# Performance work log

Measured on AMD Instinct MI355X. Metric: run time of the kernel, lower is better.

Reference implementation:

```python
import jax, jax.numpy as jnp
import numpy as np

N_NODES = 50000
N_EDGES = 800000
D = 128  # node_feat_size == edge_hidden_size


def setup_inputs() -> dict:
    key = jax.random.key(0)
    ks = jax.random.split(key, 10)
    return {
        "edge_logits": jax.random.normal(ks[0], (N_EDGES, 1), jnp.float32),
        "node_feats": jax.random.normal(ks[1], (N_NODES, D), jnp.float32),
        "src": jax.random.randint(ks[2], (N_EDGES,), 0, N_NODES),
        "dst": jax.random.randint(ks[3], (N_EDGES,), 0, N_NODES),
        "W_proj": jax.random.normal(ks[4], (D, D), jnp.float32) * 0.05,
        "b_proj": jax.random.normal(ks[5], (D,), jnp.float32) * 0.05,
        "W_ih": jax.random.normal(ks[6], (3 * D, D), jnp.float32) * 0.05,
        "b_ih": jax.random.normal(ks[7], (3 * D,), jnp.float32) * 0.05,
        "W_hh": jax.random.normal(ks[8], (3 * D, D), jnp.float32) * 0.05,
        "b_hh": jax.random.normal(ks[9], (3 * D,), jnp.float32) * 0.05,
    }


def reference(edge_logits, node_feats, src, dst, W_proj, b_proj, W_ih, b_ih, W_hh, b_hh):
    N = node_feats.shape[0]
    # --- edge softmax: normalize logits over incoming edges of each dst node ---
    emax = jax.ops.segment_max(edge_logits, dst, num_segments=N)      # [N,1]
    ex = jnp.exp(edge_logits - emax[dst])                             # [E,1]
    esum = jax.ops.segment_sum(ex, dst, num_segments=N)               # [N,1]
    a = ex / esum[dst]                                                # [E,1]
    # --- project nodes (dropout=0 -> identity), gather-multiply-scatter ---
    hv = node_feats @ W_proj.T + b_proj                               # [N,D]
    msg = hv[src] * a                                                 # [E,D]
    c = jax.ops.segment_sum(msg, dst, num_segments=N)                 # [N,D]
    context = jax.nn.elu(c)
    # --- GRUCell(input=context, hidden=node_feats), torch semantics ---
    gi = context @ W_ih.T + b_ih                                      # [N,3D]
    gh = node_feats @ W_hh.T + b_hh                                   # [N,3D]
    i_r, i_z, i_n = jnp.split(gi, 3, axis=-1)
    h_r, h_z, h_n = jnp.split(gh, 3, axis=-1)
    r = jax.nn.sigmoid(i_r + h_r)
    z = jax.nn.sigmoid(i_z + h_z)
    n = jnp.tanh(i_n + r * h_n)
    h_new = (1.0 - z) * n + z * node_feats
    return jax.nn.relu(h_new)
```

## Files before the change

### kernel.cpp

```cpp
#include <hip/hip_runtime.h>
#include <hip/hip_fp16.h>
#include <math.h>

#define NN 50000
#define NE 800000
#define DD 128
#define SLOT 64
#define NXCD 8
#define DRANGE 6250
#define FILLB 1568
#define WPREP 578
#define NFCONV 6250

typedef short bf16x8 __attribute__((ext_vector_type(8)));
typedef float f32x4 __attribute__((ext_vector_type(4)));

#define GLOAD_LDS16(gp, lp) \
    __builtin_amdgcn_global_load_lds((const __attribute__((address_space(1))) void*)(gp), \
                                     (__attribute__((address_space(3))) void*)(lp), 16, 0, 0)

__device__ __forceinline__ unsigned short f2bf(float x) {
    unsigned u = __float_as_uint(x);
    unsigned r = (u + 0x7FFFu + ((u >> 16) & 1u)) >> 16;
    return (unsigned short)r;
}
__device__ __forceinline__ float bf2f(unsigned short b) {
    return __uint_as_float(((unsigned)b) << 16);
}
__device__ __forceinline__ unsigned pack2(float x, float y) {
    return (unsigned)f2bf(x) | ((unsigned)f2bf(y) << 16);
}
__device__ __forceinline__ unsigned short f2h(float x) {
    _Float16 h = (_Float16)x;
    return *reinterpret_cast<unsigned short*>(&h);
}
__device__ __forceinline__ float h2f(unsigned short u) {
    _Float16 h = *reinterpret_cast<_Float16*>(&u);
    return (float)h;
}
__device__ __forceinline__ float fsig(float x) { return 1.f / (1.f + __expf(-x)); }
__device__ __forceinline__ float ftanh(float x) { return 1.f - 2.f / (__expf(2.f * x) + 1.f); }

__device__ __forceinline__ float wbig_val(const float* Wih, const float* Whh, int r, int c) {
    if (r < 256)  return (c < 128) ? Wih[r * 128 + c] : Whh[r * 128 + (c - 128)];
    if (r < 384)  return (c < 128) ? Wih[r * 128 + c] : 0.f;
    return (c < 128) ? 0.f : Whh[(r - 128) * 128 + (c - 128)];
}

__device__ __forceinline__ void fill_one(const float* __restrict__ logits,
                                         const int* __restrict__ src,
                                         int* __restrict__ cnt,
                                         unsigned* __restrict__ csr,
                                         int e, int d) {
    unsigned v = (unsigned)(unsigned short)src[e] |
                 ((unsigned)f2h(__expf(logits[e])) << 16);
    int p = atomicAdd(&cnt[d], 1);
    if (p < SLOT) csr[(size_t)d * SLOT + p] = v;
}

__global__ __launch_bounds__(256) void k_prepfill(const float* __restrict__ logits,
                                                  const int* __restrict__ src,
                                                  const int* __restrict__ dst,
                                                  int* __restrict__ cnt,
                                                  unsigned* __restrict__ csr,
                                                  const float* __restrict__ Wp,
                                                  const float* __restrict__ Wih,
                                                  const float* __restrict__ bih,
                                                  const float* __restrict__ Whh,
                                                  const float* __restrict__ bhh,
                                                  const float* __restrict__ nf,
                                                  unsigned short* __restrict__ Wfrag,
                                                  unsigned short* __restrict__ Wpfrag,
                                                  float* __restrict__ bbig,
                                                  unsigned* __restrict__ nfb) {
    if (blockIdx.x < FILLB) {
        const int g = blockIdx.x & 7;
        const int chunk = blockIdx.x >> 3;
        const int dlo = g * DRANGE;
        const int dhi = min(dlo + DRANGE, NN);
#pragma unroll
        for (int i = 0; i < 4; i++) {
            int e4 = chunk * 4096 + i * 1024 + (int)threadIdx.x * 4;
            if (e4 + 3 < NE) {
                int4 d = *(const int4*)(dst + e4);
                if (d.x >= dlo && d.x < dhi) fill_one(logits, src, cnt, csr, e4 + 0, d.x);
                if (d.y >= dlo && d.y < dhi) fill_one(logits, src, cnt, csr, e4 + 1, d.y);
                if (d.z >= dlo && d.z < dhi) fill_one(logits, src, cnt, csr, e4 + 2, d.z);
                if (d.w >= dlo && d.w < dhi) fill_one(logits, src, cnt, csr, e4 + 3, d.w);
            } else {
                for (int k = 0; k < 4; k++) {
                    int e = e4 + k;
                    if (e < NE) {
                        int dd = dst[e];
                        if (dd >= dlo && dd < dhi) fill_one(logits, src, cnt, csr, e, dd);
                    }
                }
            }
        }
    } else if (blockIdx.x < FILLB + WPREP) {
        int idx = (blockIdx.x - FILLB) * 256 + threadIdx.x;
        if (idx < 512 * 256) {
            int e = idx & 7, lane = (idx >> 3) & 63, ct = (idx >> 9) & 31, ks = idx >> 14;
            int r = ct * 16 + (lane & 15);
            int k = ks * 32 + (lane >> 4) * 8 + e;
            Wfrag[idx] = f2bf(wbig_val(Wih, Whh, r, k));
        } else if (idx < 512 * 256 + 128 * 128) {
            int i = idx - 512 * 256;
            int e = i & 7, lane = (i >> 3) & 63, ct = (i >> 9) & 7, ks = i >> 12;
            int r = ct * 16 + (lane & 15);
            int k = ks * 32 + (lane >> 4) * 8 + e;
            Wpfrag[i] = f2bf(Wp[r * 128 + k]);
        } else if (idx < 512 * 256 + 128 * 128 + 512) {
            int j = idx - (512 * 256 + 128 * 128);
            float v;
            if (j < 256)      v = bih[j] + bhh[j];
            else if (j < 384) v = bih[j];
            else              v = bhh[j - 128];
            bbig[j] = v;
        }
    } else {
        int t = (blockIdx.x - FILLB - WPREP) * 256 + threadIdx.x;
        float4 v = ((const float4*)nf)[t];
        nfb[t * 2 + 0] = pack2(v.x, v.y);
        nfb[t * 2 + 1] = pack2(v.z, v.w);
    }
}

__global__ __launch_bounds__(256, 2) void k_proj(const unsigned short* __restrict__ nfb,
                                                 const unsigned short* __restrict__ Wpfrag,
                                                 const float* __restrict__ bp,
                                                 unsigned short* __restrict__ hvb) {
    __shared__ unsigned short Bs[2][8 * 64 * 8];
    const int t = threadIdx.x;
    const int w = t >> 6;
    const int lane = t & 63;
    const int row0 = blockIdx.x * 64 + w * 16;
    const int rowA = min(row0 + (lane & 15), NN - 1);
    const int koff = (lane >> 4) * 8;

    bf16x8 a[4];
#pragma unroll
    for (int ks = 0; ks < 4; ks++)
        a[ks] = *reinterpret_cast<const bf16x8*>(nfb + (size_t)rowA * DD + ks * 32 + koff);

    f32x4 acc[8];
#pragma unroll
    for (int i = 0; i < 8; i++) acc[i] = (f32x4){0.f, 0.f, 0.f, 0.f};

#pragma unroll
    for (int i = 0; i < 2; i++)
        GLOAD_LDS16(Wpfrag + (size_t)(i * 256 + t) * 8, &Bs[0][(i * 256 + t) * 8]);
    __syncthreads();

#pragma unroll
    for (int ks = 0; ks < 4; ks++) {
        const int cur = ks & 1;
        if (ks < 3) {
#pragma unroll
            for (int i = 0; i < 2; i++)
                GLOAD_LDS16(Wpfrag + (size_t)(ks + 1) * 4096 + (i * 256 + t) * 8,
                            &Bs[cur ^ 1][(i * 256 + t) * 8]);
        }
#pragma unroll
        for (int ct = 0; ct < 8; ct++) {
            bf16x8 b = *reinterpret_cast<const bf16x8*>(&Bs[cur][(ct * 64 + lane) * 8]);
            acc[ct] = __builtin_amdgcn_mfma_f32_16x16x32_bf16(a[ks], b, acc[ct], 0, 0, 0);
        }
        __syncthreads();
    }
#pragma unroll
    for (int ct = 0; ct < 8; ct++) {
        int j = ct * 16 + (lane & 15);
        float bj = bp[j];
#pragma unroll
        for (int reg = 0; reg < 4; reg++) {
            int row = row0 + (lane >> 4) * 4 + reg;
            if (row < NN) hvb[(size_t)row * DD + j] = f2bf(acc[ct][reg] + bj);
        }
    }
}

__global__ __launch_bounds__(256) void k_aggr(const int* __restrict__ cnt,
                                              const unsigned* __restrict__ csr,
                                              const unsigned* __restrict__ hvb,
                                              unsigned* __restrict__ ctx_out) {
    const int n = blockIdx.x * 4 + (threadIdx.x >> 6);
    const int l = threadIdx.x & 63;
    const int beg = n * SLOT;
    const int deg = min(cnt[n], SLOT);
    const int end = beg + deg;
    float ax = 0.f, ay = 0.f, es = 0.f;
    int e = beg;
    for (; e + 8 <= end; e += 8) {
        unsigned c0 = csr[e + 0], c1 = csr[e + 1], c2 = csr[e + 2], c3 = csr[e + 3];
        unsigned c4 = csr[e + 4], c5 = csr[e + 5], c6 = csr[e + 6], c7 = csr[e + 7];
        unsigned h0 = hvb[(size_t)(c0 & 0xFFFF) * 64 + l];
        unsigned h1 = hvb[(size_t)(c1 & 0xFFFF) * 64 + l];
        unsigned h2 = hvb[(size_t)(c2 & 0xFFFF) * 64 + l];
        unsigned h3 = hvb[(size_t)(c3 & 0xFFFF) * 64 + l];
        unsigned h4 = hvb[(size_t)(c4 & 0xFFFF) * 64 + l];
        unsigned h5 = hvb[(size_t)(c5 & 0xFFFF) * 64 + l];
        unsigned h6 = hvb[(size_t)(c6 & 0xFFFF) * 64 + l];
        unsigned h7 = hvb[(size_t)(c7 & 0xFFFF) * 64 + l];
        float a0 = h2f((unsigned short)(c0 >> 16)), a1 = h2f((unsigned short)(c1 >> 16));
        float a2 = h2f((unsigned short)(c2 >> 16)), a3 = h2f((unsigned short)(c3 >> 16));
        float a4 = h2f((unsigned short)(c4 >> 16)), a5 = h2f((unsigned short)(c5 >> 16));
        float a6 = h2f((unsigned short)(c6 >> 16)), a7 = h2f((unsigned short)(c7 >> 16));
        es += ((a0 + a1) + (a2 + a3)) + ((a4 + a5) + (a6 + a7));
        ax += a0 * bf2f((unsigned short)(h0 & 0xFFFF));
        ay += a0 * bf2f((unsigned short)(h0 >> 16));
        ax += a1 * bf2f((unsigned short)(h1 & 0xFFFF));
        ay += a1 * bf2f((unsigned short)(h1 >> 16));
        ax += a2 * bf2f((unsigned short)(h2 & 0xFFFF));
        ay += a2 * bf2f((unsigned short)(h2 >> 16));
        ax += a3 * bf2f((unsigned short)(h3 & 0xFFFF));
        ay += a3 * bf2f((unsigned short)(h3 >> 16));
        ax += a4 * bf2f((unsigned short)(h4 & 0xFFFF));
        ay += a4 * bf2f((unsigned short)(h4 >> 16));
        ax += a5 * bf2f((unsigned short)(h5 & 0xFFFF));
        ay += a5 * bf2f((unsigned short)(h5 >> 16));
        ax += a6 * bf2f((unsigned short)(h6 & 0xFFFF));
        ay += a6 * bf2f((unsigned short)(h6 >> 16));
        ax += a7 * bf2f((unsigned short)(h7 & 0xFFFF));
        ay += a7 * bf2f((unsigned short)(h7 >> 16));
    }
    for (; e < end; e++) {
        unsigned c = csr[e];
        float a = h2f((unsigned short)(c >> 16));
        unsigned hv2 = hvb[(size_t)(c & 0xFFFF) * 64 + l];
        es += a;
        ax += a * bf2f((unsigned short)(hv2 & 0xFFFF));
        ay += a * bf2f((unsigned short)(hv2 >> 16));
    }
    float vx = 0.f, vy = 0.f;
    if (deg > 0) {
        float inv = 1.f / es;
        vx = ax * inv; vy = ay * inv;
        vx = vx > 0.f ? vx : expm1f(vx);
        vy = vy > 0.f ? vy : expm1f(vy);
    }
    ctx_out[(size_t)n * 128 + l] = pack2(vx, vy);
}

__global__ __launch_bounds__(256, 2) void k_gru(const unsigned short* __restrict__ nfb,
                                                const unsigned short* __restrict__ Wfrag,
                                                const float* __restrict__ bbig,
                                                float* __restrict__ out) {
    __shared__ unsigned short Bs[2][4 * 4 * 64 * 8];
    const int t = threadIdx.x;
    const int w = t >> 6;
    const int lane = t & 63;
    const int jblk = blockIdx.x & 1;
    const int row0 = (blockIdx.x >> 1) * 64 + w * 16;
    const int rowA = min(row0 + (lane & 15), NN - 1);
    const int koff = (lane >> 4) * 8;
    const unsigned short* ctxo = (const unsigned short*)out;

    bf16x8 a[8];
#pragma unroll
    for (int ks = 0; ks < 4; ks++)
        a[ks] = *reinterpret_cast<const bf16x8*>(ctxo + (size_t)rowA * 256 + ks * 32 + koff);
#pragma unroll
    for (int ks = 0; ks < 4; ks++)
        a[4 + ks] = *reinterpret_cast<const bf16x8*>(nfb + (size_t)rowA * DD + ks * 32 + koff);

    f32x4 acc[16];
#pragma unroll
    for (int i = 0; i < 16; i++) acc[i] = (f32x4){0.f, 0.f, 0.f, 0.f};

#pragma unroll
    for (int g = 0; g < 4; g++)
        GLOAD_LDS16(Wfrag + (size_t)(g * 8 + jblk * 4) * 512 + t * 8,
                    &Bs[0][g * 2048 + t * 8]);
    __syncthreads();

#pragma unroll
    for (int ks = 0; ks < 8; ks++) {
        const int cur = ks & 1;
        if (ks < 7) {
#pragma unroll
            for (int g = 0; g < 4; g++)
                GLOAD_LDS16(Wfrag + (size_t)(ks + 1) * 16384 +
                                (size_t)(g * 8 + jblk * 4) * 512 + t * 8,
                            &Bs[cur ^ 1][g * 2048 + t * 8]);
        }
#pragma unroll
        for (int q = 0; q < 16; q++) {
            bf16x8 b = *reinterpret_cast<const bf16x8*>(&Bs[cur][q * 512 + lane * 8]);
            acc[q] = __builtin_amdgcn_mfma_f32_16x16x32_bf16(a[ks], b, acc[q], 0, 0, 0);
        }
        __syncthreads();
    }

#pragma unroll
    for (int ctl = 0; ctl < 4; ctl++) {
        int j = jblk * 64 + ctl * 16 + (lane & 15);
        float bR = bbig[j];
        float bZ = bbig[128 + j];
        float bI = bbig[256 + j];
        float bH = bbig[384 + j];
#pragma unroll
        for (int reg = 0; reg < 4; reg++) {
            int row = row0 + (lane >> 4) * 4 + reg;
            if (row < NN) {
                float r = fsig(acc[ctl][reg] + bR);
                float z = fsig(acc[4 + ctl][reg] + bZ);
                float nn = ftanh(acc[8 + ctl][reg] + bI + r * (acc[12 + ctl][reg] + bH));
                float hp = bf2f(nfb[(size_t)row * DD + j]);
                float h = (1.f - z) * nn + z * hp;
                out[(size_t)row * DD + j] = fmaxf(h, 0.f);
            }
        }
    }
}

extern "C" void kernel_launch(void* const* d_in, const int* in_sizes, int n_in,
                              void* d_out, int out_size, void* d_ws, size_t ws_size,
                              hipStream_t stream) {
    const float* edge_logits = (const float*)d_in[0];
    const float* node_feats  = (const float*)d_in[1];
    const int*   src         = (const int*)d_in[2];
    const int*   dst         = (const int*)d_in[3];
    const float* Wp          = (const float*)d_in[4];
    const float* bp          = (const float*)d_in[5];
    const float* Wih         = (const float*)d_in[6];
    const float* bih         = (const float*)d_in[7];
    const float* Whh         = (const float*)d_in[8];
    const float* bhh         = (const float*)d_in[9];
    float* out = (float*)d_out;

    char* ws = (char*)d_ws;
    int*            cnt     = (int*)(ws);
    float*          bbig    = (float*)(ws + 512 * 1024);
    unsigned short* Wpfrag  = (unsigned short*)(ws + 1024 * 1024);
    unsigned short* Wfrag   = (unsigned short*)(ws + 1024 * 1024 + 64 * 1024);
    unsigned*       csr     = (unsigned*)(ws + 2 * 1024 * 1024);
    unsigned short* hvb     = (unsigned short*)(ws + 15 * 1024 * 1024);
    unsigned short* nfb     = (unsigned short*)(ws + 28 * 1024 * 1024);

    hipMemsetAsync(cnt, 0, NN * sizeof(int), stream);

    k_prepfill<<<FILLB + WPREP + NFCONV, 256, 0, stream>>>(
        edge_logits, src, dst, cnt, csr,
        Wp, Wih, bih, Whh, bhh, node_feats,
        Wfrag, Wpfrag, bbig, (unsigned*)nfb);
    k_proj<<<(NN + 63) / 64, 256, 0, stream>>>((const unsigned short*)nfb, Wpfrag, bp, hvb);
    k_aggr<<<NN / 4, 256, 0, stream>>>(cnt, csr, (const unsigned*)hvb, (unsigned*)out);
    k_gru<<<((NN + 63) / 64) * 2, 256, 0, stream>>>((const unsigned short*)nfb, Wfrag, bbig, out);
}
```

Measured before the change: 132.7 us.

## Fuse CSR fill with projection GEMM, fold memset into weight prep, remap aggregation

Weight fragment preparation and zeroing of the count array move into a small standalone kernel, which replaces the memset. The edge-bucket fill and the projection GEMM now run as two block ranges of one kernel, and the GEMM converts fp32 node features to bf16 inline, storing the bf16 copy for the GRU. This removes the separate conversion pass and one launch. The aggregation kernel maps its blocks onto the same XCD dst ranges used by the fill and gathers in batches of 16 edges with a 4-edge tail, aiming for better L2 locality and more loads in flight. The cost is an extra kernel launch for weight prep and more register pressure in the aggregation loop.

Result: faster. 128.9 us (-2.9%).

```diff
diff --git a/kernel.cpp b/kernel.cpp
--- a/kernel.cpp
+++ b/kernel.cpp
@@ -9,11 +9,12 @@
 #define NXCD 8
 #define DRANGE 6250
 #define FILLB 1568
-#define WPREP 578
-#define NFCONV 6250
+#define PROJB 782
+#define AGGR_IDX 1563
 
 typedef short bf16x8 __attribute__((ext_vector_type(8)));
 typedef float f32x4 __attribute__((ext_vector_type(4)));
+typedef unsigned uint4v __attribute__((ext_vector_type(4)));
 
 #define GLOAD_LDS16(gp, lp) \
     __builtin_amdgcn_global_load_lds((const __attribute__((address_space(1))) void*)(gp), \
@@ -45,6 +46,38 @@
     if (r < 256)  return (c < 128) ? Wih[r * 128 + c] : Whh[r * 128 + (c - 128)];
     if (r < 384)  return (c < 128) ? Wih[r * 128 + c] : 0.f;
     return (c < 128) ? 0.f : Whh[(r - 128) * 128 + (c - 128)];
+}
+
+__global__ __launch_bounds__(256) void k_wprep(const float* __restrict__ Wp,
+                                               const float* __restrict__ Wih,
+                                               const float* __restrict__ bih,
+                                               const float* __restrict__ Whh,
+                                               const float* __restrict__ bhh,
+                                               int* __restrict__ cnt,
+                                               unsigned short* __restrict__ Wfrag,
+                                               unsigned short* __restrict__ Wpfrag,
+                                               float* __restrict__ bbig) {
+    int idx = blockIdx.x * 256 + threadIdx.x;
+    if (idx < NN) cnt[idx] = 0;
+    if (idx < 512 * 256) {
+        int e = idx & 7, lane = (idx >> 3) & 63, ct = (idx >> 9) & 31, ks = idx >> 14;
+        int r = ct * 16 + (lane & 15);
+        int k = ks * 32 + (lane >> 4) * 8 + e;
+        Wfrag[idx] = f2bf(wbig_val(Wih, Whh, r, k));
+    } else if (idx < 512 * 256 + 128 * 128) {
+        int i = idx - 512 * 256;
+        int e = i & 7, lane = (i >> 3) & 63, ct = (i >> 9) & 7, ks = i >> 12;
+        int r = ct * 16 + (lane & 15);
+        int k = ks * 32 + (lane >> 4) * 8 + e;
+        Wpfrag[i] = f2bf(Wp[r * 128 + k]);
+    } else if (idx < 512 * 256 + 128 * 128 + 512) {
+        int j = idx - (512 * 256 + 128 * 128);
+        float v;
+        if (j < 256)      v = bih[j] + bhh[j];
+        else if (j < 384) v = bih[j];
+        else              v = bhh[j - 128];
+        bbig[j] = v;
+    }
 }
 
 __device__ __forceinline__ void fill_one(const float* __restrict__ logits,
@@ -58,21 +91,17 @@
     if (p < SLOT) csr[(size_t)d * SLOT + p] = v;
 }
 
-__global__ __launch_bounds__(256) void k_prepfill(const float* __restrict__ logits,
-                                                  const int* __restrict__ src,
-                                                  const int* __restrict__ dst,
-                                                  int* __restrict__ cnt,
-                                                  unsigned* __restrict__ csr,
-                                                  const float* __restrict__ Wp,
-                                                  const float* __restrict__ Wih,
-                                                  const float* __restrict__ bih,
-                                                  const float* __restrict__ Whh,
-                                                  const float* __restrict__ bhh,
-                                                  const float* __restrict__ nf,
-                                                  unsigned short* __restrict__ Wfrag,
-                                                  unsigned short* __restrict__ Wpfrag,
-                                                  float* __restrict__ bbig,
-                                                  unsigned* __restrict__ nfb) {
+__global__ __launch_bounds__(256, 2) void k_fillproj(const float* __restrict__ logits,
+                                                     const int* __restrict__ src,
+                                                     const int* __restrict__ dst,
+                                                     int* __restrict__ cnt,
+                                                     unsigned* __restrict__ csr,
+                                                     const float* __restrict__ nf,
+                                                     const unsigned short* __restrict__ Wpfrag,
+                                                     const float* __restrict__ bp,
+                                                     unsigned short* __restrict__ hvb,
+                                                     unsigned short* __restrict__ nfb) {
+    __shared__ unsigned short Bs[2][8 * 64 * 8];
     if (blockIdx.x < FILLB) {
         const int g = blockIdx.x & 7;
         const int chunk = blockIdx.x >> 3;
@@ -97,51 +126,27 @@
                 }
             }
         }
-    } else if (blockIdx.x < FILLB + WPREP) {
-        int idx = (blockIdx.x - FILLB) * 256 + threadIdx.x;
-        if (idx < 512 * 256) {
-            int e = idx & 7, lane = (idx >> 3) & 63, ct = (idx >> 9) & 31, ks = idx >> 14;
-            int r = ct * 16 + (lane & 15);
-            int k = ks * 32 + (lane >> 4) * 8 + e;
-            Wfrag[idx] = f2bf(wbig_val(Wih, Whh, r, k));
-        } else if (idx < 512 * 256 + 128 * 128) {
-            int i = idx - 512 * 256;
-            int e = i & 7, lane = (i >> 3) & 63, ct = (i >> 9) & 7, ks = i >> 12;
-            int r = ct * 16 + (lane & 15);
-            int k = ks * 32 + (lane >> 4) * 8 + e;
-            Wpfrag[i] = f2bf(Wp[r * 128 + k]);
-        } else if (idx < 512 * 256 + 128 * 128 + 512) {
-            int j = idx - (512 * 256 + 128 * 128);
-            float v;
-            if (j < 256)      v = bih[j] + bhh[j];
-            else if (j < 384) v = bih[j];
-            else              v = bhh[j - 128];
-            bbig[j] = v;
-        }
-    } else {
-        int t = (blockIdx.x - FILLB - WPREP) * 256 + threadIdx.x;
-        float4 v = ((const float4*)nf)[t];
-        nfb[t * 2 + 0] = pack2(v.x, v.y);
-        nfb[t * 2 + 1] = pack2(v.z, v.w);
-    }
-}
-
-__global__ __launch_bounds__(256, 2) void k_proj(const unsigned short* __restrict__ nfb,
-                                                 const unsigned short* __restrict__ Wpfrag,
-                                                 const float* __restrict__ bp,
-                                                 unsigned short* __restrict__ hvb) {
-    __shared__ unsigned short Bs[2][8 * 64 * 8];
+        return;
+    }
+    const int bid = blockIdx.x - FILLB;
     const int t = threadIdx.x;
     const int w = t >> 6;
     const int lane = t & 63;
-    const int row0 = blockIdx.x * 64 + w * 16;
+    const int row0 = bid * 64 + w * 16;
     const int rowA = min(row0 + (lane & 15), NN - 1);
     const int koff = (lane >> 4) * 8;
 
     bf16x8 a[4];
 #pragma unroll
-    for (int ks = 0; ks < 4; ks++)
-        a[ks] = *reinterpret_cast<const bf16x8*>(nfb + (size_t)rowA * DD + ks * 32 + koff);
+    for (int ks = 0; ks < 4; ks++) {
+        const float* p = nf + (size_t)rowA * DD + ks * 32 + koff;
+        float4 v0 = *(const float4*)(p);
+        float4 v1 = *(const float4*)(p + 4);
+        uint4v pk = {pack2(v0.x, v0.y), pack2(v0.z, v0.w),
+                     pack2(v1.x, v1.y), pack2(v1.z, v1.w)};
+        *reinterpret_cast<uint4v*>(nfb + (size_t)rowA * DD + ks * 32 + koff) = pk;
+        a[ks] = *reinterpret_cast<bf16x8*>(&pk);
+    }
 
     f32x4 acc[8];
 #pragma unroll
@@ -184,45 +189,43 @@
                                               const unsigned* __restrict__ csr,
                                               const unsigned* __restrict__ hvb,
                                               unsigned* __restrict__ ctx_out) {
-    const int n = blockIdx.x * 4 + (threadIdx.x >> 6);
+    const int g = blockIdx.x & 7;
+    const int idx = blockIdx.x >> 3;
+    const int n = g * DRANGE + idx * 4 + (threadIdx.x >> 6);
     const int l = threadIdx.x & 63;
+    if (n >= (g + 1) * DRANGE || n >= NN) return;
     const int beg = n * SLOT;
     const int deg = min(cnt[n], SLOT);
     const int end = beg + deg;
     float ax = 0.f, ay = 0.f, es = 0.f;
     int e = beg;
-    for (; e + 8 <= end; e += 8) {
-        unsigned c0 = csr[e + 0], c1 = csr[e + 1], c2 = csr[e + 2], c3 = csr[e + 3];
-        unsigned c4 = csr[e + 4], c5 = csr[e + 5], c6 = csr[e + 6], c7 = csr[e + 7];
-        unsigned h0 = hvb[(size_t)(c0 & 0xFFFF) * 64 + l];
-        unsigned h1 = hvb[(size_t)(c1 & 0xFFFF) * 64 + l];
-        unsigned h2 = hvb[(size_t)(c2 & 0xFFFF) * 64 + l];
-        unsigned h3 = hvb[(size_t)(c3 & 0xFFFF) * 64 + l];
-        unsigned h4 = hvb[(size_t)(c4 & 0xFFFF) * 64 + l];
-        unsigned h5 = hvb[(size_t)(c5 & 0xFFFF) * 64 + l];
-        unsigned h6 = hvb[(size_t)(c6 & 0xFFFF) * 64 + l];
-        unsigned h7 = hvb[(size_t)(c7 & 0xFFFF) * 64 + l];
-        float a0 = h2f((unsigned short)(c0 >> 16)), a1 = h2f((unsigned short)(c1 >> 16));
-        float a2 = h2f((unsigned short)(c2 >> 16)), a3 = h2f((unsigned short)(c3 >> 16));
-        float a4 = h2f((unsigned short)(c4 >> 16)), a5 = h2f((unsigned short)(c5 >> 16));
-        float a6 = h2f((unsigned short)(c6 >> 16)), a7 = h2f((unsigned short)(c7 >> 16));
-        es += ((a0 + a1) + (a2 + a3)) + ((a4 + a5) + (a6 + a7));
-        ax += a0 * bf2f((unsigned short)(h0 & 0xFFFF));
-        ay += a0 * bf2f((unsigned short)(h0 >> 16));
-        ax += a1 * bf2f((unsigned short)(h1 & 0xFFFF));
-        ay += a1 * bf2f((unsigned short)(h1 >> 16));
-        ax += a2 * bf2f((unsigned short)(h2 & 0xFFFF));
-        ay += a2 * bf2f((unsigned short)(h2 >> 16));
-        ax += a3 * bf2f((unsigned short)(h3 & 0xFFFF));
-        ay += a3 * bf2f((unsigned short)(h3 >> 16));
-        ax += a4 * bf2f((unsigned short)(h4 & 0xFFFF));
-        ay += a4 * bf2f((unsigned short)(h4 >> 16));
-        ax += a5 * bf2f((unsigned short)(h5 & 0xFFFF));
-        ay += a5 * bf2f((unsigned short)(h5 >> 16));
-        ax += a6 * bf2f((unsigned short)(h6 & 0xFFFF));
-        ay += a6 * bf2f((unsigned short)(h6 >> 16));
-        ax += a7 * bf2f((unsigned short)(h7 & 0xFFFF));
-        ay += a7 * bf2f((unsigned short)(h7 >> 16));
+    for (; e + 16 <= end; e += 16) {
+        unsigned c[16], h[16];
+#pragma unroll
+        for (int i = 0; i < 16; i++) c[i] = csr[e + i];
+#pragma unroll
+        for (int i = 0; i < 16; i++) h[i] = hvb[(size_t)(c[i] & 0xFFFF) * 64 + l];
+#pragma unroll
+        for (int i = 0; i < 16; i++) {
+            float a = h2f((unsigned short)(c[i] >> 16));
+            es += a;
+            ax += a * bf2f((unsigned short)(h[i] & 0xFFFF));
+            ay += a * bf2f((unsigned short)(h[i] >> 16));
+        }
+    }
+    for (; e + 4 <= end; e += 4) {
+        unsigned c[4], h[4];
+#pragma unroll
+        for (int i = 0; i < 4; i++) c[i] = csr[e + i];
+#pragma unroll
+        for (int i = 0; i < 4; i++) h[i] = hvb[(size_t)(c[i] & 0xFFFF) * 64 + l];
+#pragma unroll
+        for (int i = 0; i < 4; i++) {
+            float a = h2f((unsigned short)(c[i] >> 16));
+            es += a;
+            ax += a * bf2f((unsigned short)(h[i] & 0xFFFF));
+            ay += a * bf2f((unsigned short)(h[i] >> 16));
+        }
     }
     for (; e < end; e++) {
         unsigned c = csr[e];
@@ -338,13 +341,9 @@
     unsigned short* hvb     = (unsigned short*)(ws + 15 * 1024 * 1024);
     unsigned short* nfb     = (unsigned short*)(ws + 28 * 1024 * 1024);
 
-    hipMemsetAsync(cnt, 0, NN * sizeof(int), stream);
-
-    k_prepfill<<<FILLB + WPREP + NFCONV, 256, 0, stream>>>(
-        edge_logits, src, dst, cnt, csr,
-        Wp, Wih, bih, Whh, bhh, node_feats,
-        Wfrag, Wpfrag, bbig, (unsigned*)nfb);
-    k_proj<<<(NN + 63) / 64, 256, 0, stream>>>((const unsigned short*)nfb, Wpfrag, bp, hvb);
-    k_aggr<<<NN / 4, 256, 0, stream>>>(cnt, csr, (const unsigned*)hvb, (unsigned*)out);
+    k_wprep<<<578, 256, 0, stream>>>(Wp, Wih, bih, Whh, bhh, cnt, Wfrag, Wpfrag, bbig);
+    k_fillproj<<<FILLB + PROJB, 256, 0, stream>>>(
+        edge_logits, src, dst, cnt, csr, node_feats, Wpfrag, bp, hvb, nfb);
+    k_aggr<<<NXCD * AGGR_IDX, 256, 0, stream>>>(cnt, csr, (const unsigned*)hvb, (unsigned*)out);
     k_gru<<<((NN + 63) / 64) * 2, 256, 0, stream>>>((const unsigned short*)nfb, Wfrag, bbig, out);
 }
```
